# Kernel tuning notes

Measured on AMD Instinct MI355X. Metric: run time of the kernel, lower is better.

Reference implementation:

```python
import jax, jax.numpy as jnp
import numpy as np

N_NODES = 50000
N_EDGES = 800000
HIDDEN = 64
RES = 0.5  # args.res_layer


def setup_inputs() -> dict:
    key = jax.random.key(0)
    ks = jax.random.split(key, 9)
    s = 0.05  # scale weights to keep exp(att) stable
    return {
        "edge_index": jax.random.randint(ks[0], (2, N_EDGES), 0, N_NODES, dtype=jnp.int32),
        "adj_values": jax.random.uniform(ks[1], (N_EDGES,), dtype=jnp.float32),
        "embeds": jax.random.normal(ks[2], (N_NODES, HIDDEN), dtype=jnp.float32),
        "W1": jax.random.normal(ks[3], (HIDDEN, HIDDEN), dtype=jnp.float32) * s,
        "b1": jax.random.normal(ks[4], (HIDDEN,), dtype=jnp.float32) * s,
        "W2": jax.random.normal(ks[5], (HIDDEN, HIDDEN), dtype=jnp.float32) * s,
        "b2": jax.random.normal(ks[6], (HIDDEN,), dtype=jnp.float32) * s,
        "att_w": jax.random.normal(ks[7], (2 * HIDDEN,), dtype=jnp.float32) * s,
        "att_b": jax.random.normal(ks[8], (1,), dtype=jnp.float32) * s,
    }


def reference(edge_index, adj_values, embeds, W1, b1, W2, b2, att_w, att_b):
    n = embeds.shape[0]
    h = embeds.shape[1]
    row, col = edge_index[0], edge_index[1]
    # per-edge gather + two small linears with ReLU
    f1 = jax.nn.relu(embeds[row] @ W1 + b1)          # [E, h]
    f2 = jax.nn.relu(embeds[col] @ W2 + b2)          # [E, h]
    # attention score = Linear(concat(f1, f2)) -> split weight, avoid concat
    att = f1 @ att_w[:h] + f2 @ att_w[h:] + att_b[0]  # [E]
    exp_att = jnp.exp(att)
    # sparse row-wise softmax denominator via segment sum
    rowsum = jax.ops.segment_sum(exp_att, row, num_segments=n) + 1e-6  # [N]
    values = (exp_att / rowsum[row] + RES * adj_values) / (1.0 + RES)  # [E]
    # SpMM: out[i] = sum_{e: row[e]=i} values[e] * embeds[col[e]]
    out = jax.ops.segment_sum(values[:, None] * embeds[col], row, num_segments=n)  # [N, h]
    return values, out
```

## Files before the change

kernel.cpp:

```cpp
#include <hip/hip_runtime.h>
#include <hip/hip_bf16.h>

#define HID 64
#define RES_F 0.5f
#define NBKT 196
#define BCAP 5120
#define EB   256
#define LCAP 48

typedef __attribute__((ext_vector_type(8))) short short8;
typedef __attribute__((ext_vector_type(4))) float f32x4;

__device__ __forceinline__ float lane_bcast_f(float v, int k) {
    return __builtin_bit_cast(float, __builtin_amdgcn_readlane(__builtin_bit_cast(int, v), k));
}
__device__ __forceinline__ int lane_bcast_i(int v, int k) {
    return __builtin_amdgcn_readlane(v, k);
}
__device__ __forceinline__ short f2bf(float x) {
    __hip_bfloat16 h = __float2bfloat16(x);
    return __builtin_bit_cast(short, h);
}

__global__ void __launch_bounds__(256) fused_prep_kernel(
    const float* __restrict__ embeds,
    const float* __restrict__ W1, const float* __restrict__ W2,
    const float* __restrict__ b1, const float* __restrict__ b2,
    const float* __restrict__ att_w, const float* __restrict__ att_b,
    const int* __restrict__ row, const int* __restrict__ col,
    const float* __restrict__ adj,
    int2* __restrict__ bstream, int* __restrict__ bcnt,
    float* __restrict__ g, float* __restrict__ corr,
    __hip_bfloat162* __restrict__ embeds_bf,
    int n, int E, int nodeBlocks)
{
    __shared__ short sW[2 * HID * HID];

    if (blockIdx.x < nodeBlocks) {
        for (int i = threadIdx.x; i < HID * HID; i += blockDim.x) {
            sW[i]             = f2bf(W1[i]);
            sW[HID * HID + i] = f2bf(W2[i]);
        }
        __syncthreads();

        const float ab = att_b[0];
        const int lane = threadIdx.x & 63;
        const int colx = lane & 15;
        const int quad = lane >> 4;

        short8 bfrag[8][2];
        float  sac[8], bc[8];
#pragma unroll
        for (int cb = 0; cb < 8; ++cb) {
            const int jp = cb * 16 + colx;
            const short* w = (jp < HID) ? (sW + jp) : (sW + HID * HID + jp - HID);
#pragma unroll
            for (int kh = 0; kh < 2; ++kh) {
                short8 f;
#pragma unroll
                for (int j = 0; j < 8; ++j) {
                    const int k = kh * 32 + quad * 8 + j;
                    f[j] = w[k * HID];
                }
                bfrag[cb][kh] = f;
            }
            sac[cb] = att_w[jp];
            bc[cb]  = (jp < HID) ? b1[jp] : b2[jp - HID];
        }

        int gwave = (blockIdx.x * blockDim.x + threadIdx.x) >> 6;
        const int nwave = (nodeBlocks * blockDim.x) >> 6;
        const int nbatch = (n + 15) >> 4;

        for (int b = gwave; b < nbatch; b += nwave) {
            const int base = b << 4;
            int mrow = base + colx;
            if (mrow >= n) mrow = n - 1;
            const float* ep = embeds + (size_t)mrow * HID;
            short8 afrag0, afrag1;
#pragma unroll
            for (int j = 0; j < 8; ++j) {
                afrag0[j] = f2bf(ep[quad * 8 + j]);
                afrag1[j] = f2bf(ep[32 + quad * 8 + j]);
            }

            float acc1[4] = {0.f, 0.f, 0.f, 0.f};
            float acc2[4] = {0.f, 0.f, 0.f, 0.f};
#pragma unroll
            for (int cb = 0; cb < 8; ++cb) {
                f32x4 C = {0.f, 0.f, 0.f, 0.f};
                C = __builtin_amdgcn_mfma_f32_16x16x32_bf16(afrag0, bfrag[cb][0], C, 0, 0, 0);
                C = __builtin_amdgcn_mfma_f32_16x16x32_bf16(afrag1, bfrag[cb][1], C, 0, 0, 0);
#pragma unroll
                for (int reg = 0; reg < 4; ++reg) {
                    const float v = fmaxf(C[reg] + bc[cb], 0.f) * sac[cb];
                    if (cb < 4) acc1[reg] += v; else acc2[reg] += v;
                }
            }
#pragma unroll
            for (int reg = 0; reg < 4; ++reg) {
#pragma unroll
                for (int off = 1; off < 16; off <<= 1) {
                    acc1[reg] += __shfl_xor(acc1[reg], off, 64);
                    acc2[reg] += __shfl_xor(acc2[reg], off, 64);
                }
            }
            if (colx == 0) {
#pragma unroll
                for (int reg = 0; reg < 4; ++reg) {
                    const int i = base + quad * 4 + reg;
                    if (i < n) {
                        g[i]    = __expf(acc2[reg]);
                        corr[i] = 1e-6f * __expf(-(acc1[reg] + ab));
                    }
                }
            }
        }
    } else {
        int* lcnt = (int*)sW;
        for (int k = threadIdx.x; k < NBKT; k += 256) lcnt[k] = 0;
        __syncthreads();

        const int eb  = blockIdx.x - nodeBlocks;
        const int tid = eb * 256 + threadIdx.x;
        const int ts  = EB * 256;

        const float2* ef2 = (const float2*)embeds;
        const int npair = n * (HID / 2);
        for (int i = tid; i < npair; i += ts) {
            float2 f = ef2[i];
            __hip_bfloat162 h;
            h.x = __float2bfloat16(f.x);
            h.y = __float2bfloat16(f.y);
            embeds_bf[i] = h;
        }

        const int chunk = (E + EB - 1) / EB;
        const int e0 = eb * chunk;
        const int e1 = min(E, e0 + chunk);
        for (int e = e0 + (int)threadIdx.x; e < e1; e += 256) {
            const int r    = row[e];
            const int c    = col[e];
            const float aj = adj[e];
            const unsigned aq = (unsigned)(aj * 65535.0f + 0.5f);
            const int k = r >> 8;
            const int2 pl = make_int2((int)((unsigned)c | (aq << 16)),
                                      (r & 255) | (e << 8));
            const int pos = atomicAdd(&lcnt[k], 1);
            if (pos < LCAP)
                bstream[((size_t)k * EB + eb) * LCAP + pos] = pl;
        }
        __syncthreads();

        for (int k = threadIdx.x; k < NBKT; k += 256)
            bcnt[eb * NBKT + k] = min(lcnt[k], LCAP);
    }
}

__global__ void __launch_bounds__(256) regroup_kernel(
    const int2* __restrict__ bstream, const int* __restrict__ bcnt,
    int2* __restrict__ edata2, int* __restrict__ rowdir, int n)
{
    __shared__ int cnt[256], scan[256], wcur[256];
    const int k = blockIdx.x;
    const int t = threadIdx.x;
    cnt[t] = 0;
    const int myc = bcnt[t * NBKT + k];
    __syncthreads();

    const int2* src = bstream + ((size_t)k * EB + t) * LCAP;
    for (int j = 0; j < myc; ++j)
        atomicAdd(&cnt[src[j].y & 255], 1);
    __syncthreads();

    scan[t] = cnt[t];
    __syncthreads();
    for (int ofs = 1; ofs < 256; ofs <<= 1) {
        const int v = (t >= ofs) ? scan[t - ofs] : 0;
        __syncthreads();
        scan[t] += v;
        __syncthreads();
    }
    const int excl = scan[t] - cnt[t];
    wcur[t] = excl;
    const int r = k * 256 + t;
    if (r < n)
        rowdir[r] = (k * BCAP + excl) | (min(cnt[t], 64) << 20);
    __syncthreads();

    int2* dst = edata2 + (size_t)k * BCAP;
    for (int j = 0; j < myc; ++j) {
        const int2 pl = src[j];
        const int p = atomicAdd(&wcur[pl.y & 255], 1);
        dst[p] = pl;
    }
}

__global__ void __launch_bounds__(256) spmm_kernel(
    const int* __restrict__ rowdir, const int2* __restrict__ edata2,
    const __hip_bfloat16* __restrict__ embeds_bf,
    const float* __restrict__ g, const float* __restrict__ corr,
    float* __restrict__ values, float* __restrict__ out, int n)
{
    const float inv = 1.0f / (1.0f + RES_F);
    const int lane = threadIdx.x & 63;
    int r = (blockIdx.x * blockDim.x + threadIdx.x) >> 6;
    const int nwave = (gridDim.x * blockDim.x) >> 6;

    for (; r < n; r += nwave) {
        const int pk    = rowdir[r];
        const int start = pk & 0xFFFFF;
        const int deg   = pk >> 20;
        const bool valid = lane < deg;
        int c = 0, e = 0;
        float gc = 0.0f, aj = 0.0f;
        if (valid) {
            const int2 ed = edata2[(size_t)start + lane];
            const unsigned pk0 = (unsigned)ed.x;
            c  = (int)(pk0 & 0xFFFFu);
            aj = (float)(pk0 >> 16) * (1.0f / 65535.0f);
            e  = (int)(((unsigned)ed.y) >> 8);
            gc = g[c];
        }
        float G = gc;
#pragma unroll
        for (int off = 1; off < 64; off <<= 1)
            G += __shfl_xor(G, off, 64);
        const float invDr = 1.0f / (G + corr[r]);
        float v = 0.0f;
        if (valid) {
            v = (gc * invDr + RES_F * aj) * inv;
            values[e] = v;
        }

        float acc = 0.0f;
        int j = 0;
        for (; j + 8 <= deg; j += 8) {
            const int   c0 = lane_bcast_i(c, j + 0);
            const int   c1 = lane_bcast_i(c, j + 1);
            const int   c2 = lane_bcast_i(c, j + 2);
            const int   c3 = lane_bcast_i(c, j + 3);
            const int   c4 = lane_bcast_i(c, j + 4);
            const int   c5 = lane_bcast_i(c, j + 5);
            const int   c6 = lane_bcast_i(c, j + 6);
            const int   c7 = lane_bcast_i(c, j + 7);
            const float b0 = __bfloat162float(embeds_bf[c0 * HID + lane]);
            const float b1 = __bfloat162float(embeds_bf[c1 * HID + lane]);
            const float b2 = __bfloat162float(embeds_bf[c2 * HID + lane]);
            const float b3 = __bfloat162float(embeds_bf[c3 * HID + lane]);
            const float b4 = __bfloat162float(embeds_bf[c4 * HID + lane]);
            const float b5 = __bfloat162float(embeds_bf[c5 * HID + lane]);
            const float b6 = __bfloat162float(embeds_bf[c6 * HID + lane]);
            const float b7 = __bfloat162float(embeds_bf[c7 * HID + lane]);
            acc = fmaf(lane_bcast_f(v, j + 0), b0, acc);
            acc = fmaf(lane_bcast_f(v, j + 1), b1, acc);
            acc = fmaf(lane_bcast_f(v, j + 2), b2, acc);
            acc = fmaf(lane_bcast_f(v, j + 3), b3, acc);
            acc = fmaf(lane_bcast_f(v, j + 4), b4, acc);
            acc = fmaf(lane_bcast_f(v, j + 5), b5, acc);
            acc = fmaf(lane_bcast_f(v, j + 6), b6, acc);
            acc = fmaf(lane_bcast_f(v, j + 7), b7, acc);
        }
        for (; j < deg; ++j) {
            const int   cj = lane_bcast_i(c, j);
            const float vj = lane_bcast_f(v, j);
            acc = fmaf(vj, __bfloat162float(embeds_bf[cj * HID + lane]), acc);
        }
        out[r * HID + lane] = acc;
    }
}

extern "C" void kernel_launch(void* const* d_in, const int* in_sizes, int n_in,
                              void* d_out, int out_size, void* d_ws, size_t ws_size,
                              hipStream_t stream_)
{
    const int* edge_index = (const int*)d_in[0];
    const float* adj      = (const float*)d_in[1];
    const float* embeds   = (const float*)d_in[2];
    const float* W1       = (const float*)d_in[3];
    const float* b1       = (const float*)d_in[4];
    const float* W2       = (const float*)d_in[5];
    const float* b2       = (const float*)d_in[6];
    const float* att_w    = (const float*)d_in[7];
    const float* att_b    = (const float*)d_in[8];

    const int E = in_sizes[1];
    const int N = in_sizes[2] / HID;

    const int* row = edge_index;
    const int* col = edge_index + E;

    int2*  bstream = (int2*)d_ws;
    int2*  edata2  = bstream + (size_t)NBKT * EB * LCAP;
    int*   bcnt    = (int*)(edata2 + (size_t)NBKT * BCAP);
    int*   rowdir  = bcnt + EB * NBKT;
    float* g       = (float*)(rowdir + N);
    float* corr    = g + N;
    __hip_bfloat16* embeds_bf = (__hip_bfloat16*)(corr + N);

    float* values = (float*)d_out;
    float* out    = values + E;

    const int nodeBlocks = 512;
    fused_prep_kernel<<<nodeBlocks + EB, 256, 0, stream_>>>(
        embeds, W1, W2, b1, b2, att_w, att_b, row, col, adj,
        bstream, bcnt, g, corr, (__hip_bfloat162*)embeds_bf,
        N, E, nodeBlocks);

    regroup_kernel<<<NBKT, 256, 0, stream_>>>(bstream, bcnt, edata2, rowdir, N);

    spmm_kernel<<<12544, 256, 0, stream_>>>(rowdir, edata2, embeds_bf,
                                            g, corr, values, out, N);
}
```

Measured before the change: 151.6 us.

## Fuse bf16 embedding conversion into node MFMA pass; split SpMM gather across half-waves

The fp32-to-bf16 conversion of embeds no longer runs as a separate loop in the edge blocks. The node blocks now write the bf16 rows straight from the MFMA A-fragments they already build, so embeds is read once instead of twice. In the SpMM kernel each half-wave handles alternate edges and each lane loads a bf16 pair, which halves the number of gather instructions per edge; a cross-half shuffle then reduces the two halves and stores the result as float2. The trade-off is that ds_bpermute-based shuffles replace the scalar readlane broadcasts, which adds some LDS latency per edge.

New measurement: 144.5 us. 1.05x faster.

```diff
diff --git a/kernel.cpp b/kernel.cpp
--- a/kernel.cpp
+++ b/kernel.cpp
@@ -14,12 +14,12 @@
 __device__ __forceinline__ float lane_bcast_f(float v, int k) {
     return __builtin_bit_cast(float, __builtin_amdgcn_readlane(__builtin_bit_cast(int, v), k));
 }
-__device__ __forceinline__ int lane_bcast_i(int v, int k) {
-    return __builtin_amdgcn_readlane(v, k);
-}
 __device__ __forceinline__ short f2bf(float x) {
     __hip_bfloat16 h = __float2bfloat16(x);
     return __builtin_bit_cast(short, h);
+}
+__device__ __forceinline__ float bf2f(unsigned short u) {
+    return __builtin_bit_cast(float, ((unsigned)u) << 16);
 }
 
 __global__ void __launch_bounds__(256) fused_prep_kernel(
@@ -31,7 +31,7 @@
     const float* __restrict__ adj,
     int2* __restrict__ bstream, int* __restrict__ bcnt,
     float* __restrict__ g, float* __restrict__ corr,
-    __hip_bfloat162* __restrict__ embeds_bf,
+    __hip_bfloat16* __restrict__ embeds_bf,
     int n, int E, int nodeBlocks)
 {
     __shared__ short sW[2 * HID * HID];
@@ -82,6 +82,11 @@
             for (int j = 0; j < 8; ++j) {
                 afrag0[j] = f2bf(ep[quad * 8 + j]);
                 afrag1[j] = f2bf(ep[32 + quad * 8 + j]);
+            }
+            {
+                short8* ebf = (short8*)(embeds_bf + (size_t)mrow * HID);
+                ebf[quad]     = afrag0;
+                ebf[4 + quad] = afrag1;
             }
 
             float acc1[4] = {0.f, 0.f, 0.f, 0.f};
@@ -121,20 +126,7 @@
         for (int k = threadIdx.x; k < NBKT; k += 256) lcnt[k] = 0;
         __syncthreads();
 
-        const int eb  = blockIdx.x - nodeBlocks;
-        const int tid = eb * 256 + threadIdx.x;
-        const int ts  = EB * 256;
-
-        const float2* ef2 = (const float2*)embeds;
-        const int npair = n * (HID / 2);
-        for (int i = tid; i < npair; i += ts) {
-            float2 f = ef2[i];
-            __hip_bfloat162 h;
-            h.x = __float2bfloat16(f.x);
-            h.y = __float2bfloat16(f.y);
-            embeds_bf[i] = h;
-        }
-
+        const int eb = blockIdx.x - nodeBlocks;
         const int chunk = (E + EB - 1) / EB;
         const int e0 = eb * chunk;
         const int e1 = min(E, e0 + chunk);
@@ -204,6 +196,8 @@
 {
     const float inv = 1.0f / (1.0f + RES_F);
     const int lane = threadIdx.x & 63;
+    const int half = lane >> 5;
+    const int hl   = lane & 31;
     int r = (blockIdx.x * blockDim.x + threadIdx.x) >> 6;
     const int nwave = (gridDim.x * blockDim.x) >> 6;
 
@@ -233,40 +227,42 @@
             values[e] = v;
         }
 
-        float acc = 0.0f;
+        float accx = 0.0f, accy = 0.0f;
         int j = 0;
         for (; j + 8 <= deg; j += 8) {
-            const int   c0 = lane_bcast_i(c, j + 0);
-            const int   c1 = lane_bcast_i(c, j + 1);
-            const int   c2 = lane_bcast_i(c, j + 2);
-            const int   c3 = lane_bcast_i(c, j + 3);
-            const int   c4 = lane_bcast_i(c, j + 4);
-            const int   c5 = lane_bcast_i(c, j + 5);
-            const int   c6 = lane_bcast_i(c, j + 6);
-            const int   c7 = lane_bcast_i(c, j + 7);
-            const float b0 = __bfloat162float(embeds_bf[c0 * HID + lane]);
-            const float b1 = __bfloat162float(embeds_bf[c1 * HID + lane]);
-            const float b2 = __bfloat162float(embeds_bf[c2 * HID + lane]);
-            const float b3 = __bfloat162float(embeds_bf[c3 * HID + lane]);
-            const float b4 = __bfloat162float(embeds_bf[c4 * HID + lane]);
-            const float b5 = __bfloat162float(embeds_bf[c5 * HID + lane]);
-            const float b6 = __bfloat162float(embeds_bf[c6 * HID + lane]);
-            const float b7 = __bfloat162float(embeds_bf[c7 * HID + lane]);
-            acc = fmaf(lane_bcast_f(v, j + 0), b0, acc);
-            acc = fmaf(lane_bcast_f(v, j + 1), b1, acc);
-            acc = fmaf(lane_bcast_f(v, j + 2), b2, acc);
-            acc = fmaf(lane_bcast_f(v, j + 3), b3, acc);
-            acc = fmaf(lane_bcast_f(v, j + 4), b4, acc);
-            acc = fmaf(lane_bcast_f(v, j + 5), b5, acc);
-            acc = fmaf(lane_bcast_f(v, j + 6), b6, acc);
-            acc = fmaf(lane_bcast_f(v, j + 7), b7, acc);
-        }
-        for (; j < deg; ++j) {
-            const int   cj = lane_bcast_i(c, j);
-            const float vj = lane_bcast_f(v, j);
-            acc = fmaf(vj, __bfloat162float(embeds_bf[cj * HID + lane]), acc);
-        }
-        out[r * HID + lane] = acc;
+            const int j0 = j + half,     j1 = j + 2 + half;
+            const int j2 = j + 4 + half, j3 = j + 6 + half;
+            const int   c0 = __shfl(c, j0, 64);
+            const int   c1 = __shfl(c, j1, 64);
+            const int   c2 = __shfl(c, j2, 64);
+            const int   c3 = __shfl(c, j3, 64);
+            const float v0 = __shfl(v, j0, 64);
+            const float v1 = __shfl(v, j1, 64);
+            const float v2 = __shfl(v, j2, 64);
+            const float v3 = __shfl(v, j3, 64);
+            const ushort2 h0 = *(const ushort2*)(embeds_bf + (size_t)c0 * HID + hl * 2);
+            const ushort2 h1 = *(const ushort2*)(embeds_bf + (size_t)c1 * HID + hl * 2);
+            const ushort2 h2 = *(const ushort2*)(embeds_bf + (size_t)c2 * HID + hl * 2);
+            const ushort2 h3 = *(const ushort2*)(embeds_bf + (size_t)c3 * HID + hl * 2);
+            accx = fmaf(v0, bf2f(h0.x), accx); accy = fmaf(v0, bf2f(h0.y), accy);
+            accx = fmaf(v1, bf2f(h1.x), accx); accy = fmaf(v1, bf2f(h1.y), accy);
+            accx = fmaf(v2, bf2f(h2.x), accx); accy = fmaf(v2, bf2f(h2.y), accy);
+            accx = fmaf(v3, bf2f(h3.x), accx); accy = fmaf(v3, bf2f(h3.y), accy);
+        }
+        for (; j < deg; j += 2) {
+            const int j0 = j + half;
+            const int   cj = __shfl(c, j0, 64);
+            const float vj = __shfl(v, j0, 64);
+            const ushort2 h = *(const ushort2*)(embeds_bf + (size_t)cj * HID + hl * 2);
+            accx = fmaf(vj, bf2f(h.x), accx);
+            accy = fmaf(vj, bf2f(h.y), accy);
+        }
+        accx += __shfl_xor(accx, 32, 64);
+        accy += __shfl_xor(accy, 32, 64);
+        if (lane < 32) {
+            float2 o; o.x = accx; o.y = accy;
+            ((float2*)(out + (size_t)r * HID))[hl] = o;
+        }
     }
 }
 
@@ -304,7 +300,7 @@
     const int nodeBlocks = 512;
     fused_prep_kernel<<<nodeBlocks + EB, 256, 0, stream_>>>(
         embeds, W1, W2, b1, b2, att_w, att_b, row, col, adj,
-        bstream, bcnt, g, corr, (__hip_bfloat162*)embeds_bf,
+        bstream, bcnt, g, corr, embeds_bf,
         N, E, nodeBlocks);
 
     regroup_kernel<<<NBKT, 256, 0, stream_>>>(bstream, bcnt, edata2, rowdir, N);
```
